# Kernel optimization log

Hardware: AMD Instinct MI355X
Metric: run time of the kernel (lower is better)

The kernel has to match this reference:

```python
import jax, jax.numpy as jnp
import numpy as np

BEV_H, BEV_W = 200, 200
X_RANGE = (-50.0, 50.0)
Y_RANGE = (-50.0, 50.0)
IMG_W, IMG_H = 1600.0, 928.0
EPS = 1e-6


def _bev_points():
    x_half = (X_RANGE[1] - X_RANGE[0]) / (2 * BEV_W)
    y_half = (Y_RANGE[1] - Y_RANGE[0]) / (2 * BEV_H)
    xs = jnp.linspace(X_RANGE[0] + x_half, X_RANGE[1] - x_half, BEV_W)
    ys = jnp.linspace(Y_RANGE[0] + y_half, Y_RANGE[1] - y_half, BEV_H)
    gy, gx = jnp.meshgrid(ys, xs, indexing='ij')
    return jnp.stack([gx, gy, jnp.zeros_like(gx)], -1).reshape(-1, 3)  # (P,3)


def _bilinear_zeros(fm, x, y):
    # fm: (C,H,W); x,y: (P,) pixel coords; grid_sample bilinear, zeros padding, align_corners=True
    H, W = fm.shape[1], fm.shape[2]
    x0 = jnp.floor(x); y0 = jnp.floor(y)
    wx = x - x0; wy = y - y0
    def g(xi, yi):
        ok = ((xi >= 0) & (xi <= W - 1) & (yi >= 0) & (yi <= H - 1)).astype(fm.dtype)
        xc = jnp.clip(xi, 0, W - 1).astype(jnp.int32)
        yc = jnp.clip(yi, 0, H - 1).astype(jnp.int32)
        return fm[:, yc, xc] * ok  # (C,P)
    v00 = g(x0, y0); v01 = g(x0 + 1, y0); v10 = g(x0, y0 + 1); v11 = g(x0 + 1, y0 + 1)
    return v00 * (1 - wx) * (1 - wy) + v01 * wx * (1 - wy) + v10 * (1 - wx) * wy + v11 * wx * wy


def _bev_forward(feats, intrinsics, extrinsics, conv_w, conv_b, bn_gamma, bn_beta, bn_mean, bn_var):
    B, N, C, fH, fW = feats.shape
    pts = _bev_points()                                   # (P,3), z=0 ground plane
    E = jnp.linalg.inv(extrinsics)                        # T_ego->cam (B,N,4,4)
    R = E[..., :3, :3]; t = E[..., :3, 3]
    pts_cam = jnp.einsum('bnij,pj->bnpi', R, pts) + t[:, :, None, :]  # (B,N,P,3)
    depth = pts_cam[..., 2]
    p_img = jnp.einsum('bnij,bnpj->bnpi', intrinsics, pts_cam)
    u = p_img[..., 0] / (p_img[..., 2] + EPS)
    v = p_img[..., 1] / (p_img[..., 2] + EPS)
    u_feat = u * (fW / IMG_W); v_feat = v * (fH / IMG_H)
    u_norm = u_feat / (fW - 1.0) * 2.0 - 1.0
    v_norm = v_feat / (fH - 1.0) * 2.0 - 1.0
    valid = ((depth > 0.1) & (u_norm >= -1.0) & (u_norm <= 1.0)
             & (v_norm >= -1.0) & (v_norm <= 1.0)).astype(feats.dtype)  # (B,N,P)
    # align_corners=True: pixel coords recover u_feat/v_feat
    xs = (u_norm + 1.0) * 0.5 * (fW - 1.0)
    ys = (v_norm + 1.0) * 0.5 * (fH - 1.0)
    P = BEV_H * BEV_W
    bev_sum = jnp.zeros((B, C, P), feats.dtype)
    valid_sum = jnp.zeros((B, 1, P), feats.dtype)
    sample_b = jax.vmap(_bilinear_zeros)
    for cam in range(N):  # small fixed camera loop, as in original
        s = sample_b(feats[:, cam], xs[:, cam], ys[:, cam])  # (B,C,P)
        vb = valid[:, cam][:, None, :]
        bev_sum = bev_sum + s * vb
        valid_sum = valid_sum + vb
    bev = (bev_sum / (valid_sum + EPS)).reshape(B, C, BEV_H, BEV_W)
    # 1x1 conv + inference BatchNorm + ReLU
    y = jnp.einsum('oc,bchw->bohw', conv_w, bev) + conv_b[:, None, None]
    y = (y - bn_mean[:, None, None]) / jnp.sqrt(bn_var[:, None, None] + 1e-5)
    y = y * bn_gamma[:, None, None] + bn_beta[:, None, None]
    return jax.nn.relu(y)


def setup_inputs() -> dict:
    key = jax.random.key(0)
    ks = jax.random.split(key, 6)
    B, N, C, fH, fW = 4, 6, 256, 29, 50
    feats = jax.random.normal(ks[0], (B, N, C, fH, fW), jnp.float32)
    # intrinsics: realistic pinhole K
    fx = 1266.0 + 20.0 * jax.random.normal(ks[1], (B, N), jnp.float32)
    fy = 1266.0 + 20.0 * jax.random.normal(ks[2], (B, N), jnp.float32)
    z = jnp.zeros((B, N), jnp.float32); o = jnp.ones((B, N), jnp.float32)
    K = jnp.stack([jnp.stack([fx, z, 800.0 * o], -1),
                   jnp.stack([z, fy, 464.0 * o], -1),
                   jnp.stack([z, z, o], -1)], -2)  # (B,N,3,3)
    # extrinsics: proper SE(3) T_cam->ego (random rotation via QR + translation)
    A = jax.random.normal(ks[3], (B, N, 3, 3), jnp.float32)
    Q, _ = jnp.linalg.qr(A)
    Q = jnp.where(jnp.linalg.det(Q)[..., None, None] < 0, -Q, Q)
    tr = jax.random.uniform(ks[4], (B, N, 3), jnp.float32, -2.0, 2.0)
    E = jnp.zeros((B, N, 4, 4), jnp.float32)
    E = E.at[..., :3, :3].set(Q).at[..., :3, 3].set(tr).at[..., 3, 3].set(1.0)
    conv_w = 0.05 * jax.random.normal(ks[5], (C, C), jnp.float32)
    return {
        'feats': feats, 'intrinsics': K, 'extrinsics': E,
        'conv_w': conv_w, 'conv_b': jnp.zeros((C,), jnp.float32),
        'bn_gamma': jnp.ones((C,), jnp.float32), 'bn_beta': jnp.zeros((C,), jnp.float32),
        'bn_mean': jnp.zeros((C,), jnp.float32), 'bn_var': jnp.ones((C,), jnp.float32),
    }


def reference(feats, intrinsics, extrinsics, conv_w, conv_b, bn_gamma, bn_beta, bn_mean, bn_var):
    return _bev_forward(feats, intrinsics, extrinsics, conv_w, conv_b,
                        bn_gamma, bn_beta, bn_mean, bn_var)
```

## Files before the change

kernel.cpp:

```cpp
#include <hip/hip_runtime.h>
#include <hip/hip_bf16.h>


#define P_TOT  40000
#define FH     29
#define FW     50
#define NCAM   6

typedef short bf16x8 __attribute__((ext_vector_type(8)));
typedef float f32x4  __attribute__((ext_vector_type(4)));
typedef unsigned short u16x8 __attribute__((ext_vector_type(8)));

__device__ __forceinline__ float bf2f(unsigned short u) {
    union { unsigned int i; float f; } x; x.i = ((unsigned int)u) << 16; return x.f;
}
__device__ __forceinline__ unsigned short f2bf(float f) {
    union { float f; unsigned int i; } x; x.f = f;
    unsigned int i = x.i;
    return (unsigned short)((i + 0x7FFFu + ((i >> 16) & 1u)) >> 16);
}

__global__ __launch_bounds__(256) void prep_transpose_kernel(
        const float* __restrict__ feats, const float* __restrict__ K,
        const float* __restrict__ E, const float* __restrict__ convw,
        const float* __restrict__ convb, const float* __restrict__ gamma,
        const float* __restrict__ beta, const float* __restrict__ mean,
        const float* __restrict__ var, float* __restrict__ params,
        float* __restrict__ sb, unsigned short* __restrict__ wbf,
        unsigned short* __restrict__ ft) {
    __shared__ unsigned short tile[256][58];
    int blk = blockIdx.x;
    int t   = threadIdx.x;
    if (blk < 256) {
        int idx = blk * 256 + t;
        wbf[idx] = f2bf(convw[idx]);
    }
    if (blk == 696) {
        int o = t;
        float rstd = rsqrtf(var[o] + 1e-5f);
        float s = gamma[o] * rstd;
        sb[o]       = s;
        sb[256 + o] = (convb[o] - mean[o]) * s + beta[o];
        if (o >= 24) return;
        const float* e = E + o * 16;
        const float* k = K + o * 9;
        float a00=e[0], a01=e[1], a02=e[2],  t0=e[3];
        float a10=e[4], a11=e[5], a12=e[6],  t1=e[7];
        float a20=e[8], a21=e[9], a22=e[10], t2=e[11];
        float c00 =  (a11*a22 - a12*a21);
        float c01 = -(a10*a22 - a12*a20);
        float c02 =  (a10*a21 - a11*a20);
        float det = a00*c00 + a01*c01 + a02*c02;
        float id = 1.0f / det;
        float i00 =  c00*id;
        float i01 = -(a01*a22 - a02*a21)*id;
        float i02 =  (a01*a12 - a02*a11)*id;
        float i10 =  c01*id;
        float i11 =  (a00*a22 - a02*a20)*id;
        float i12 = -(a00*a12 - a02*a10)*id;
        float i20 =  c02*id;
        float i21 = -(a00*a21 - a01*a20)*id;
        float i22 =  (a00*a11 - a01*a10)*id;
        float tp0 = -(i00*t0 + i01*t1 + i02*t2);
        float tp1 = -(i10*t0 + i11*t1 + i12*t2);
        float tp2 = -(i20*t0 + i21*t1 + i22*t2);
        float* q = params + o * 12;
        q[0] = k[0]*i00 + k[1]*i10 + k[2]*i20;
        q[1] = k[0]*i01 + k[1]*i11 + k[2]*i21;
        q[2] = k[0]*tp0 + k[1]*tp1 + k[2]*tp2;
        q[3] = k[3]*i00 + k[4]*i10 + k[5]*i20;
        q[4] = k[3]*i01 + k[4]*i11 + k[5]*i21;
        q[5] = k[3]*tp0 + k[4]*tp1 + k[5]*tp2;
        q[6] = k[6]*i00 + k[7]*i10 + k[8]*i20;
        q[7] = k[6]*i01 + k[7]*i11 + k[8]*i21;
        q[8] = k[6]*tp0 + k[7]*tp1 + k[8]*tp2;
        q[9]  = i20;
        q[10] = i21;
        q[11] = tp2;
        return;
    }
    int bn = blk / FH, y = blk - bn * FH;
    const float* src = feats + (size_t)bn * 256 * FH * FW + y * FW;
    #pragma unroll
    for (int i = 0; i < 25; ++i) {
        int flat = i * 512 + t * 2;
        int c = flat / 50;
        int x = flat - c * 50;
        float2 v = *(const float2*)(src + c * FH * FW + x);
        tile[c][x]     = f2bf(v.x);
        tile[c][x + 1] = f2bf(v.y);
    }
    __syncthreads();
    unsigned short* dst = ft + (size_t)blk * 50 * 256;
    #pragma unroll
    for (int i = 0; i < 25; ++i) {
        int flat = i * 512 + t * 2;
        int x = flat >> 8;
        int c = flat & 255;
        unsigned int v = (unsigned int)tile[c][x] | ((unsigned int)tile[c + 1][x] << 16);
        *(unsigned int*)(dst + x * 256 + c) = v;
    }
}

__global__ __launch_bounds__(512, 4) void fused_kernel(const unsigned short* __restrict__ ft,
                                                       const float* __restrict__ params,
                                                       const unsigned short* __restrict__ wbf,
                                                       const float* __restrict__ sb,
                                                       float* __restrict__ out) {
    __shared__ unsigned short Bt[64][264];
    __shared__ int           sbf[64][6];
    __shared__ unsigned int  swxy[64][6];
    __shared__ int           scnt[64];
    __shared__ float         sscale[64];
    __shared__ float         ssb[512];

    int tid   = threadIdx.x;
    int pbase = blockIdx.x * 64;
    int b     = blockIdx.y;

    ssb[tid] = sb[tid];

    if (tid < 384) {
        int pt  = tid / 6;
        int cam = tid - pt * 6;
        int p   = pbase + pt;
        float gx = -49.75f + 0.5f * (float)(p % 200);
        float gy = -49.75f + 0.5f * (float)(p / 200);
        const float* q = params + (b * NCAM + cam) * 12;
        float wh    = q[6] * gx + q[7]  * gy + q[8];
        float depth = q[9] * gx + q[10] * gy + q[11];
        float inv = 1.0f / (wh + 1e-6f);
        float u = (q[0] * gx + q[1] * gy + q[2]) * inv;
        float v = (q[3] * gx + q[4] * gy + q[5]) * inv;
        float un = u * (50.0f / 1600.0f) * (2.0f / 49.0f) - 1.0f;
        float vn = v * (29.0f / 928.0f)  * (2.0f / 28.0f) - 1.0f;
        int bf = -1; unsigned int wxy = 0;
        if (depth > 0.1f && un >= -1.0f && un <= 1.0f &&
                            vn >= -1.0f && vn <= 1.0f) {
            float xs = (un + 1.0f) * 0.5f * 49.0f;
            float ys = (vn + 1.0f) * 0.5f * 28.0f;
            float x0f = floorf(xs), y0f = floorf(ys);
            float wx = xs - x0f, wy = ys - y0f;
            int x0 = (int)x0f, y0 = (int)y0f;
            int okx = (x0 < FW - 1) ? 1 : 0;
            int oky = (y0 < FH - 1) ? 2 : 0;
            int base = (((b * NCAM + cam) * FH + y0) * FW + x0) * 256;
            bf  = base | okx | oky;
            wxy = (unsigned int)(wx * 65535.0f + 0.5f)
                | ((unsigned int)(wy * 65535.0f + 0.5f) << 16);
        }
        sbf[pt][cam]  = bf;
        swxy[pt][cam] = wxy;
    }
    __syncthreads();

    if (tid < 64) {
        int c = 0;
        #pragma unroll
        for (int cam = 0; cam < NCAM; ++cam) {
            int v = sbf[tid][cam];
            unsigned int w = swxy[tid][cam];
            if (v >= 0) { sbf[tid][c] = v; swxy[tid][c] = w; ++c; }
        }
        scnt[tid]   = c;
        sscale[tid] = 1.0f / ((float)c + 1e-6f);
    }
    __syncthreads();

    {
        int pt = tid >> 3, sub = tid & 7;
        int chb = sub * 8;
        float acc[32];
        #pragma unroll
        for (int j = 0; j < 32; ++j) acc[j] = 0.0f;
        int n = scnt[pt];
        for (int s = 0; s < n; ++s) {
            int bf = sbf[pt][s];
            unsigned int wxy = swxy[pt][s];
            int base = bf & ~255;
            int okx = bf & 1, oky = bf & 2;
            float wx = (float)(wxy & 0xffffu) * (1.0f / 65535.0f);
            float wy = (float)(wxy >> 16)     * (1.0f / 65535.0f);
            float iwx = 1.0f - wx, iwy = 1.0f - wy;
            float w00 = iwx * iwy;
            float w01 = okx ? wx * iwy : 0.0f;
            float w10 = oky ? iwx * wy : 0.0f;
            float w11 = (okx && oky) ? wx * wy : 0.0f;
            const unsigned short* p00 = ft + base + chb;
            int o01 = okx ? 256 : 0;
            int o10 = oky ? FW * 256 : 0;
            #pragma unroll
            for (int qv = 0; qv < 4; ++qv) {
                u16x8 v0 = *(const u16x8*)(p00 + qv * 64);
                #pragma unroll
                for (int j = 0; j < 8; ++j) acc[qv * 8 + j] += w00 * bf2f(v0[j]);
            }
            #pragma unroll
            for (int qv = 0; qv < 4; ++qv) {
                u16x8 v1 = *(const u16x8*)(p00 + o01 + qv * 64);
                #pragma unroll
                for (int j = 0; j < 8; ++j) acc[qv * 8 + j] += w01 * bf2f(v1[j]);
            }
            #pragma unroll
            for (int qv = 0; qv < 4; ++qv) {
                u16x8 v2 = *(const u16x8*)(p00 + o10 + qv * 64);
                #pragma unroll
                for (int j = 0; j < 8; ++j) acc[qv * 8 + j] += w10 * bf2f(v2[j]);
            }
            #pragma unroll
            for (int qv = 0; qv < 4; ++qv) {
                u16x8 v3 = *(const u16x8*)(p00 + o10 + o01 + qv * 64);
                #pragma unroll
                for (int j = 0; j < 8; ++j) acc[qv * 8 + j] += w11 * bf2f(v3[j]);
            }
        }
        float sc = sscale[pt];
        #pragma unroll
        for (int qv = 0; qv < 4; ++qv) {
            u16x8 ov;
            #pragma unroll
            for (int j = 0; j < 8; ++j) ov[j] = f2bf(acc[qv * 8 + j] * sc);
            *(u16x8*)&Bt[pt][chb + qv * 64] = ov;
        }
    }
    __syncthreads();

    int lane = tid & 63, wv = tid >> 6;
    f32x4 acc2[2][4];
    #pragma unroll
    for (int f = 0; f < 2; ++f)
        #pragma unroll
        for (int nf = 0; nf < 4; ++nf) acc2[f][nf] = (f32x4){0.f, 0.f, 0.f, 0.f};
    int arow = wv * 32 + (lane & 15);
    int kq   = (lane >> 4) * 8;
    const unsigned short* wptr = wbf + arow * 256 + kq;
    #pragma unroll
    for (int kt = 0; kt < 8; ++kt) {
        bf16x8 a0 = *(const bf16x8*)(wptr + kt * 32);
        bf16x8 a1 = *(const bf16x8*)(wptr + 16 * 256 + kt * 32);
        #pragma unroll
        for (int nf = 0; nf < 4; ++nf) {
            bf16x8 bb = *(const bf16x8*)&Bt[nf * 16 + (lane & 15)][kt * 32 + kq];
            acc2[0][nf] = __builtin_amdgcn_mfma_f32_16x16x32_bf16(a0, bb, acc2[0][nf], 0, 0, 0);
            acc2[1][nf] = __builtin_amdgcn_mfma_f32_16x16x32_bf16(a1, bb, acc2[1][nf], 0, 0, 0);
        }
    }
    #pragma unroll
    for (int f = 0; f < 2; ++f) {
        #pragma unroll
        for (int nf = 0; nf < 4; ++nf) {
            #pragma unroll
            for (int r = 0; r < 4; ++r) {
                int o = wv * 32 + f * 16 + (lane >> 4) * 4 + r;
                float y = acc2[f][nf][r] * ssb[o] + ssb[256 + o];
                out[((size_t)(b * 256 + o)) * P_TOT + pbase + nf * 16 + (lane & 15)]
                    = fmaxf(y, 0.0f);
            }
        }
    }
}

extern "C" void kernel_launch(void* const* d_in, const int* in_sizes, int n_in,
                              void* d_out, int out_size, void* d_ws, size_t ws_size,
                              hipStream_t stream) {
    const float* feats = (const float*)d_in[0];
    const float* intr  = (const float*)d_in[1];
    const float* extr  = (const float*)d_in[2];
    const float* convw = (const float*)d_in[3];
    const float* convb = (const float*)d_in[4];
    const float* gamma = (const float*)d_in[5];
    const float* beta  = (const float*)d_in[6];
    const float* mean  = (const float*)d_in[7];
    const float* var   = (const float*)d_in[8];

    char* ws = (char*)d_ws;
    float*          params = (float*)(ws + 0);
    float*          sb     = (float*)(ws + 2048);
    unsigned short* wbf    = (unsigned short*)(ws + 4096);
    unsigned short* ft     = (unsigned short*)(ws + 135168);
    float* out = (float*)d_out;

    hipLaunchKernelGGL(prep_transpose_kernel, dim3(697), dim3(256), 0, stream,
                       feats, intr, extr, convw, convb, gamma, beta, mean, var,
                       params, sb, wbf, ft);
    hipLaunchKernelGGL(fused_kernel, dim3(625, 4), dim3(512), 0, stream,
                       ft, params, wbf, sb, out);
}
```

Before: 76.87 us.

## Apply 1x1 conv to feature texels before bilinear BEV sampling

Because the sampling, averaging and 1x1 conv are all linear, the conv is now applied once per camera feature texel in a separate MFMA GEMM kernel. That covers about 35k texels instead of 160k BEV points. A combine kernel then bilinearly gathers the conv outputs per output channel, applies the visibility average, BN scale/bias and ReLU, and writes float4 chunks. The goal is to cut matrix-multiply work and the per-point 256-channel gathers. In exchange it adds an extra kernel launch, a bf16 intermediate buffer (an extra rounding step), scalar per-channel gathers, and less contiguous output writes per wavefront.

```diff
diff --git a/kernel.cpp b/kernel.cpp
--- a/kernel.cpp
+++ b/kernel.cpp
@@ -6,10 +6,11 @@
 #define FH     29
 #define FW     50
 #define NCAM   6
+#define NTEX   34800
+#define NTEXP  34816
 
 typedef short bf16x8 __attribute__((ext_vector_type(8)));
 typedef float f32x4  __attribute__((ext_vector_type(4)));
-typedef unsigned short u16x8 __attribute__((ext_vector_type(8)));
 
 __device__ __forceinline__ float bf2f(unsigned short u) {
     union { unsigned int i; float f; } x; x.i = ((unsigned int)u) << 16; return x.f;
@@ -102,27 +103,64 @@
     }
 }
 
-__global__ __launch_bounds__(512, 4) void fused_kernel(const unsigned short* __restrict__ ft,
-                                                       const float* __restrict__ params,
-                                                       const unsigned short* __restrict__ wbf,
-                                                       const float* __restrict__ sb,
-                                                       float* __restrict__ out) {
-    __shared__ unsigned short Bt[64][264];
-    __shared__ int           sbf[64][6];
-    __shared__ unsigned int  swxy[64][6];
-    __shared__ int           scnt[64];
-    __shared__ float         sscale[64];
-    __shared__ float         ssb[512];
+__global__ __launch_bounds__(256) void gemm2_kernel(const unsigned short* __restrict__ ftm,
+                                                    const unsigned short* __restrict__ wbf,
+                                                    unsigned short* __restrict__ G) {
+    __shared__ unsigned short Ft[64][40];
+    __shared__ unsigned short Wo[64][40];
+    int texbase = blockIdx.x * 64;
+    int obase   = blockIdx.y * 64;
+    int tid  = threadIdx.x;
+    int lane = tid & 63;
+    int wv   = tid >> 6;
+    int lrow = tid >> 2;
+    int lk   = (tid & 3) * 8;
+    const unsigned short* fsrc = ftm + (size_t)(texbase + lrow) * 256 + lk;
+    const unsigned short* wsrc = wbf + (size_t)(obase + lrow) * 256 + lk;
+    f32x4 acc[4];
+    #pragma unroll
+    for (int nf = 0; nf < 4; ++nf) acc[nf] = (f32x4){0.f, 0.f, 0.f, 0.f};
+    int arow = wv * 16 + (lane & 15);
+    int kq   = (lane >> 4) * 8;
+    for (int kt = 0; kt < 8; ++kt) {
+        *(uint4*)&Ft[lrow][lk] = *(const uint4*)(fsrc + kt * 32);
+        *(uint4*)&Wo[lrow][lk] = *(const uint4*)(wsrc + kt * 32);
+        __syncthreads();
+        bf16x8 a = *(const bf16x8*)&Ft[arow][kq];
+        #pragma unroll
+        for (int nf = 0; nf < 4; ++nf) {
+            bf16x8 bb = *(const bf16x8*)&Wo[nf * 16 + (lane & 15)][kq];
+            acc[nf] = __builtin_amdgcn_mfma_f32_16x16x32_bf16(a, bb, acc[nf], 0, 0, 0);
+        }
+        __syncthreads();
+    }
+    #pragma unroll
+    for (int nf = 0; nf < 4; ++nf) {
+        int o = obase + nf * 16 + (lane & 15);
+        #pragma unroll
+        for (int r = 0; r < 4; ++r) {
+            int tex = texbase + wv * 16 + (lane >> 4) * 4 + r;
+            G[(size_t)tex * 256 + o] = f2bf(acc[nf][r]);
+        }
+    }
+}
+
+__global__ __launch_bounds__(256) void combine_kernel(const float* __restrict__ params,
+                                                      const unsigned short* __restrict__ G,
+                                                      const float* __restrict__ sb,
+                                                      float* __restrict__ out) {
+    __shared__ int    sbase[64][6];
+    __shared__ float4 swt[64][6];
+    __shared__ int    scnt[64];
+    __shared__ float  sscale[64];
 
     int tid   = threadIdx.x;
     int pbase = blockIdx.x * 64;
     int b     = blockIdx.y;
 
-    ssb[tid] = sb[tid];
-
-    if (tid < 384) {
-        int pt  = tid / 6;
-        int cam = tid - pt * 6;
+    for (int task = tid; task < 384; task += 256) {
+        int pt  = task / 6;
+        int cam = task - pt * 6;
         int p   = pbase + pt;
         float gx = -49.75f + 0.5f * (float)(p % 200);
         float gy = -49.75f + 0.5f * (float)(p / 200);
@@ -134,7 +172,8 @@
         float v = (q[3] * gx + q[4] * gy + q[5]) * inv;
         float un = u * (50.0f / 1600.0f) * (2.0f / 49.0f) - 1.0f;
         float vn = v * (29.0f / 928.0f)  * (2.0f / 28.0f) - 1.0f;
-        int bf = -1; unsigned int wxy = 0;
+        int bfv = -1;
+        float4 w4 = {0.f, 0.f, 0.f, 0.f};
         if (depth > 0.1f && un >= -1.0f && un <= 1.0f &&
                             vn >= -1.0f && vn <= 1.0f) {
             float xs = (un + 1.0f) * 0.5f * 49.0f;
@@ -145,12 +184,15 @@
             int okx = (x0 < FW - 1) ? 1 : 0;
             int oky = (y0 < FH - 1) ? 2 : 0;
             int base = (((b * NCAM + cam) * FH + y0) * FW + x0) * 256;
-            bf  = base | okx | oky;
-            wxy = (unsigned int)(wx * 65535.0f + 0.5f)
-                | ((unsigned int)(wy * 65535.0f + 0.5f) << 16);
-        }
-        sbf[pt][cam]  = bf;
-        swxy[pt][cam] = wxy;
+            bfv = base | okx | oky;
+            float iwx = 1.0f - wx, iwy = 1.0f - wy;
+            w4.x = iwx * iwy;
+            w4.y = okx ? wx * iwy : 0.0f;
+            w4.z = oky ? iwx * wy : 0.0f;
+            w4.w = (okx && oky) ? wx * wy : 0.0f;
+        }
+        sbase[pt][cam] = bfv;
+        swt[pt][cam]   = w4;
     }
     __syncthreads();
 
@@ -158,105 +200,41 @@
         int c = 0;
         #pragma unroll
         for (int cam = 0; cam < NCAM; ++cam) {
-            int v = sbf[tid][cam];
-            unsigned int w = swxy[tid][cam];
-            if (v >= 0) { sbf[tid][c] = v; swxy[tid][c] = w; ++c; }
+            int v = sbase[tid][cam];
+            float4 w = swt[tid][cam];
+            if (v >= 0) { sbase[tid][c] = v; swt[tid][c] = w; ++c; }
         }
         scnt[tid]   = c;
         sscale[tid] = 1.0f / ((float)c + 1e-6f);
     }
     __syncthreads();
 
-    {
-        int pt = tid >> 3, sub = tid & 7;
-        int chb = sub * 8;
-        float acc[32];
-        #pragma unroll
-        for (int j = 0; j < 32; ++j) acc[j] = 0.0f;
-        int n = scnt[pt];
-        for (int s = 0; s < n; ++s) {
-            int bf = sbf[pt][s];
-            unsigned int wxy = swxy[pt][s];
-            int base = bf & ~255;
-            int okx = bf & 1, oky = bf & 2;
-            float wx = (float)(wxy & 0xffffu) * (1.0f / 65535.0f);
-            float wy = (float)(wxy >> 16)     * (1.0f / 65535.0f);
-            float iwx = 1.0f - wx, iwy = 1.0f - wy;
-            float w00 = iwx * iwy;
-            float w01 = okx ? wx * iwy : 0.0f;
-            float w10 = oky ? iwx * wy : 0.0f;
-            float w11 = (okx && oky) ? wx * wy : 0.0f;
-            const unsigned short* p00 = ft + base + chb;
-            int o01 = okx ? 256 : 0;
-            int o10 = oky ? FW * 256 : 0;
-            #pragma unroll
-            for (int qv = 0; qv < 4; ++qv) {
-                u16x8 v0 = *(const u16x8*)(p00 + qv * 64);
-                #pragma unroll
-                for (int j = 0; j < 8; ++j) acc[qv * 8 + j] += w00 * bf2f(v0[j]);
+    int o = tid;
+    float so = sb[o];
+    float bo = sb[256 + o];
+    const unsigned short* Go = G + o;
+    float* op = out + ((size_t)(b * 256 + o)) * P_TOT + pbase;
+    for (int pg = 0; pg < 16; ++pg) {
+        float4 vout;
+        #pragma unroll
+        for (int j = 0; j < 4; ++j) {
+            int p = pg * 4 + j;
+            int n = scnt[p];
+            float a = 0.f;
+            for (int s = 0; s < n; ++s) {
+                int bfv  = sbase[p][s];
+                float4 w = swt[p][s];
+                const unsigned short* g0 = Go + (bfv & ~255);
+                int o01 = (bfv & 1) ? 256 : 0;
+                int o10 = (bfv & 2) ? FW * 256 : 0;
+                a += w.x * bf2f(g0[0])
+                   + w.y * bf2f(g0[o01])
+                   + w.z * bf2f(g0[o10])
+                   + w.w * bf2f(g0[o10 + o01]);
             }
-            #pragma unroll
-            for (int qv = 0; qv < 4; ++qv) {
-                u16x8 v1 = *(const u16x8*)(p00 + o01 + qv * 64);
-                #pragma unroll
-                for (int j = 0; j < 8; ++j) acc[qv * 8 + j] += w01 * bf2f(v1[j]);
-            }
-            #pragma unroll
-            for (int qv = 0; qv < 4; ++qv) {
-                u16x8 v2 = *(const u16x8*)(p00 + o10 + qv * 64);
-                #pragma unroll
-                for (int j = 0; j < 8; ++j) acc[qv * 8 + j] += w10 * bf2f(v2[j]);
-            }
-            #pragma unroll
-            for (int qv = 0; qv < 4; ++qv) {
-                u16x8 v3 = *(const u16x8*)(p00 + o10 + o01 + qv * 64);
-                #pragma unroll
-                for (int j = 0; j < 8; ++j) acc[qv * 8 + j] += w11 * bf2f(v3[j]);
-            }
-        }
-        float sc = sscale[pt];
-        #pragma unroll
-        for (int qv = 0; qv < 4; ++qv) {
-            u16x8 ov;
-            #pragma unroll
-            for (int j = 0; j < 8; ++j) ov[j] = f2bf(acc[qv * 8 + j] * sc);
-            *(u16x8*)&Bt[pt][chb + qv * 64] = ov;
-        }
-    }
-    __syncthreads();
-
-    int lane = tid & 63, wv = tid >> 6;
-    f32x4 acc2[2][4];
-    #pragma unroll
-    for (int f = 0; f < 2; ++f)
-        #pragma unroll
-        for (int nf = 0; nf < 4; ++nf) acc2[f][nf] = (f32x4){0.f, 0.f, 0.f, 0.f};
-    int arow = wv * 32 + (lane & 15);
-    int kq   = (lane >> 4) * 8;
-    const unsigned short* wptr = wbf + arow * 256 + kq;
-    #pragma unroll
-    for (int kt = 0; kt < 8; ++kt) {
-        bf16x8 a0 = *(const bf16x8*)(wptr + kt * 32);
-        bf16x8 a1 = *(const bf16x8*)(wptr + 16 * 256 + kt * 32);
-        #pragma unroll
-        for (int nf = 0; nf < 4; ++nf) {
-            bf16x8 bb = *(const bf16x8*)&Bt[nf * 16 + (lane & 15)][kt * 32 + kq];
-            acc2[0][nf] = __builtin_amdgcn_mfma_f32_16x16x32_bf16(a0, bb, acc2[0][nf], 0, 0, 0);
-            acc2[1][nf] = __builtin_amdgcn_mfma_f32_16x16x32_bf16(a1, bb, acc2[1][nf], 0, 0, 0);
-        }
-    }
-    #pragma unroll
-    for (int f = 0; f < 2; ++f) {
-        #pragma unroll
-        for (int nf = 0; nf < 4; ++nf) {
-            #pragma unroll
-            for (int r = 0; r < 4; ++r) {
-                int o = wv * 32 + f * 16 + (lane >> 4) * 4 + r;
-                float y = acc2[f][nf][r] * ssb[o] + ssb[256 + o];
-                out[((size_t)(b * 256 + o)) * P_TOT + pbase + nf * 16 + (lane & 15)]
-                    = fmaxf(y, 0.0f);
-            }
-        }
+            ((float*)&vout)[j] = fmaxf(a * sscale[p] * so + bo, 0.0f);
+        }
+        *(float4*)(op + pg * 4) = vout;
     }
 }
 
@@ -278,11 +256,14 @@
     float*          sb     = (float*)(ws + 2048);
     unsigned short* wbf    = (unsigned short*)(ws + 4096);
     unsigned short* ft     = (unsigned short*)(ws + 135168);
+    unsigned short* G      = (unsigned short*)(ws + 135168 + (size_t)NTEXP * 512);
     float* out = (float*)d_out;
 
     hipLaunchKernelGGL(prep_transpose_kernel, dim3(697), dim3(256), 0, stream,
                        feats, intr, extr, convw, convb, gamma, beta, mean, var,
                        params, sb, wbf, ft);
-    hipLaunchKernelGGL(fused_kernel, dim3(625, 4), dim3(512), 0, stream,
-                       ft, params, wbf, sb, out);
-}
+    hipLaunchKernelGGL(gemm2_kernel, dim3(NTEXP / 64, 4), dim3(256), 0, stream,
+                       ft, wbf, G);
+    hipLaunchKernelGGL(combine_kernel, dim3(625, 4), dim3(256), 0, stream,
+                       params, G, sb, out);
+}
```

Result: slower. 179.5 us (+133.6%).

## Halve BEV points per block and split bilinear corners across thread pairs

Applied to the files above, without the earlier changes.

Each block now handles 32 BEV points instead of 64, and the grid doubles to 1250x4. In the sampling stage, 16 threads share a point: each half takes one x-corner column (two loads instead of four), and the halves combine through a warp shuffle. The goal is more parallelism and memory-level concurrency for the gather-bound stage. The cost is that each block reuses the conv weights over fewer points, so the MFMA stage does half the work per weight load and more blocks reload the weights.

```diff
diff --git a/kernel.cpp b/kernel.cpp
--- a/kernel.cpp
+++ b/kernel.cpp
@@ -107,20 +107,20 @@
                                                        const unsigned short* __restrict__ wbf,
                                                        const float* __restrict__ sb,
                                                        float* __restrict__ out) {
-    __shared__ unsigned short Bt[64][264];
-    __shared__ int           sbf[64][6];
-    __shared__ unsigned int  swxy[64][6];
-    __shared__ int           scnt[64];
-    __shared__ float         sscale[64];
+    __shared__ unsigned short Bt[32][264];
+    __shared__ int           sbf[32][6];
+    __shared__ unsigned int  swxy[32][6];
+    __shared__ int           scnt[32];
+    __shared__ float         sscale[32];
     __shared__ float         ssb[512];
 
     int tid   = threadIdx.x;
-    int pbase = blockIdx.x * 64;
+    int pbase = blockIdx.x * 32;
     int b     = blockIdx.y;
 
     ssb[tid] = sb[tid];
 
-    if (tid < 384) {
+    if (tid < 192) {
         int pt  = tid / 6;
         int cam = tid - pt * 6;
         int p   = pbase + pt;
@@ -134,7 +134,7 @@
         float v = (q[3] * gx + q[4] * gy + q[5]) * inv;
         float un = u * (50.0f / 1600.0f) * (2.0f / 49.0f) - 1.0f;
         float vn = v * (29.0f / 928.0f)  * (2.0f / 28.0f) - 1.0f;
-        int bf = -1; unsigned int wxy = 0;
+        int bfv = -1; unsigned int wxy = 0;
         if (depth > 0.1f && un >= -1.0f && un <= 1.0f &&
                             vn >= -1.0f && vn <= 1.0f) {
             float xs = (un + 1.0f) * 0.5f * 49.0f;
@@ -145,16 +145,16 @@
             int okx = (x0 < FW - 1) ? 1 : 0;
             int oky = (y0 < FH - 1) ? 2 : 0;
             int base = (((b * NCAM + cam) * FH + y0) * FW + x0) * 256;
-            bf  = base | okx | oky;
+            bfv = base | okx | oky;
             wxy = (unsigned int)(wx * 65535.0f + 0.5f)
                 | ((unsigned int)(wy * 65535.0f + 0.5f) << 16);
         }
-        sbf[pt][cam]  = bf;
+        sbf[pt][cam]  = bfv;
         swxy[pt][cam] = wxy;
     }
     __syncthreads();
 
-    if (tid < 64) {
+    if (tid < 32) {
         int c = 0;
         #pragma unroll
         for (int cam = 0; cam < NCAM; ++cam) {
@@ -168,69 +168,64 @@
     __syncthreads();
 
     {
-        int pt = tid >> 3, sub = tid & 7;
-        int chb = sub * 8;
+        int pt = tid >> 4;
+        int sub = tid & 15;
+        int cp  = sub >> 3;
+        int e   = sub & 7;
+        int chb = e * 8;
         float acc[32];
         #pragma unroll
         for (int j = 0; j < 32; ++j) acc[j] = 0.0f;
         int n = scnt[pt];
+        float sc = sscale[pt];
         for (int s = 0; s < n; ++s) {
-            int bf = sbf[pt][s];
+            int bfv = sbf[pt][s];
             unsigned int wxy = swxy[pt][s];
-            int base = bf & ~255;
-            int okx = bf & 1, oky = bf & 2;
+            int base = bfv & ~255;
+            int okx = bfv & 1, oky = bfv & 2;
             float wx = (float)(wxy & 0xffffu) * (1.0f / 65535.0f);
             float wy = (float)(wxy >> 16)     * (1.0f / 65535.0f);
-            float iwx = 1.0f - wx, iwy = 1.0f - wy;
-            float w00 = iwx * iwy;
-            float w01 = okx ? wx * iwy : 0.0f;
-            float w10 = oky ? iwx * wy : 0.0f;
-            float w11 = (okx && oky) ? wx * wy : 0.0f;
-            const unsigned short* p00 = ft + base + chb;
-            int o01 = okx ? 256 : 0;
-            int o10 = oky ? FW * 256 : 0;
+            float wxs = cp ? wx : (1.0f - wx);
+            if (cp && !okx) wxs = 0.0f;
+            float iwy = 1.0f - wy;
+            float w0 = wxs * iwy;
+            float w1 = oky ? wxs * wy : 0.0f;
+            int xoff = (cp && okx) ? 256 : 0;
+            int yoff = oky ? FW * 256 : 0;
+            const unsigned short* pA = ft + base + xoff + chb;
             #pragma unroll
             for (int qv = 0; qv < 4; ++qv) {
-                u16x8 v0 = *(const u16x8*)(p00 + qv * 64);
+                u16x8 v0 = *(const u16x8*)(pA + qv * 64);
+                u16x8 v1 = *(const u16x8*)(pA + yoff + qv * 64);
                 #pragma unroll
-                for (int j = 0; j < 8; ++j) acc[qv * 8 + j] += w00 * bf2f(v0[j]);
+                for (int j = 0; j < 8; ++j)
+                    acc[qv * 8 + j] += w0 * bf2f(v0[j]) + w1 * bf2f(v1[j]);
             }
+        }
+        #pragma unroll
+        for (int j = 0; j < 32; ++j) {
+            float v = acc[j];
+            v += __shfl_xor(v, 8);
+            acc[j] = v * sc;
+        }
+        if (cp == 0) {
             #pragma unroll
             for (int qv = 0; qv < 4; ++qv) {
-                u16x8 v1 = *(const u16x8*)(p00 + o01 + qv * 64);
+                u16x8 ov;
                 #pragma unroll
-                for (int j = 0; j < 8; ++j) acc[qv * 8 + j] += w01 * bf2f(v1[j]);
+                for (int j = 0; j < 8; ++j) ov[j] = f2bf(acc[qv * 8 + j]);
+                *(u16x8*)&Bt[pt][chb + qv * 64] = ov;
             }
-            #pragma unroll
-            for (int qv = 0; qv < 4; ++qv) {
-                u16x8 v2 = *(const u16x8*)(p00 + o10 + qv * 64);
-                #pragma unroll
-                for (int j = 0; j < 8; ++j) acc[qv * 8 + j] += w10 * bf2f(v2[j]);
-            }
-            #pragma unroll
-            for (int qv = 0; qv < 4; ++qv) {
-                u16x8 v3 = *(const u16x8*)(p00 + o10 + o01 + qv * 64);
-                #pragma unroll
-                for (int j = 0; j < 8; ++j) acc[qv * 8 + j] += w11 * bf2f(v3[j]);
-            }
-        }
-        float sc = sscale[pt];
-        #pragma unroll
-        for (int qv = 0; qv < 4; ++qv) {
-            u16x8 ov;
-            #pragma unroll
-            for (int j = 0; j < 8; ++j) ov[j] = f2bf(acc[qv * 8 + j] * sc);
-            *(u16x8*)&Bt[pt][chb + qv * 64] = ov;
         }
     }
     __syncthreads();
 
     int lane = tid & 63, wv = tid >> 6;
-    f32x4 acc2[2][4];
+    f32x4 acc2[2][2];
     #pragma unroll
     for (int f = 0; f < 2; ++f)
         #pragma unroll
-        for (int nf = 0; nf < 4; ++nf) acc2[f][nf] = (f32x4){0.f, 0.f, 0.f, 0.f};
+        for (int nf = 0; nf < 2; ++nf) acc2[f][nf] = (f32x4){0.f, 0.f, 0.f, 0.f};
     int arow = wv * 32 + (lane & 15);
     int kq   = (lane >> 4) * 8;
     const unsigned short* wptr = wbf + arow * 256 + kq;
@@ -239,7 +234,7 @@
         bf16x8 a0 = *(const bf16x8*)(wptr + kt * 32);
         bf16x8 a1 = *(const bf16x8*)(wptr + 16 * 256 + kt * 32);
         #pragma unroll
-        for (int nf = 0; nf < 4; ++nf) {
+        for (int nf = 0; nf < 2; ++nf) {
             bf16x8 bb = *(const bf16x8*)&Bt[nf * 16 + (lane & 15)][kt * 32 + kq];
             acc2[0][nf] = __builtin_amdgcn_mfma_f32_16x16x32_bf16(a0, bb, acc2[0][nf], 0, 0, 0);
             acc2[1][nf] = __builtin_amdgcn_mfma_f32_16x16x32_bf16(a1, bb, acc2[1][nf], 0, 0, 0);
@@ -248,7 +243,7 @@
     #pragma unroll
     for (int f = 0; f < 2; ++f) {
         #pragma unroll
-        for (int nf = 0; nf < 4; ++nf) {
+        for (int nf = 0; nf < 2; ++nf) {
             #pragma unroll
             for (int r = 0; r < 4; ++r) {
                 int o = wv * 32 + f * 16 + (lane >> 4) * 4 + r;
@@ -283,6 +278,6 @@
     hipLaunchKernelGGL(prep_transpose_kernel, dim3(697), dim3(256), 0, stream,
                        feats, intr, extr, convw, convb, gamma, beta, mean, var,
                        params, sb, wbf, ft);
-    hipLaunchKernelGGL(fused_kernel, dim3(625, 4), dim3(512), 0, stream,
+    hipLaunchKernelGGL(fused_kernel, dim3(1250, 4), dim3(512), 0, stream,
                        ft, params, wbf, sb, out);
 }
```

New measurement: 115.3 us. 1.5x slower.
